# Kernel tuning notes

Measured on AMD Instinct MI355X. Metric: run time of the kernel, lower is better.

Reference implementation:

```python
import jax, jax.numpy as jnp
import numpy as np

B, SX, SY, D = 32, 2048, 2048, 160

def setup_inputs() -> dict:
    key = jax.random.key(0)
    ks = jax.random.split(key, 5)
    s = 1.0 / np.sqrt(D)
    return {
        "x": jax.random.normal(ks[0], (B, SX, D), dtype=jnp.float32),
        "y": jax.random.normal(ks[1], (B, SY, D), dtype=jnp.float32),
        "Wq": jax.random.normal(ks[2], (D, D), dtype=jnp.float32) * s,
        "bq": jnp.zeros((D,), dtype=jnp.float32),
        "Wk": jax.random.normal(ks[3], (D, D), dtype=jnp.float32) * s,
        "bk": jnp.zeros((D,), dtype=jnp.float32),
        "Wv": jax.random.normal(ks[4], (D, D), dtype=jnp.float32) * s,
        "bv": jnp.zeros((D,), dtype=jnp.float32),
    }

def reference(x, y, Wq, bq, Wk, bk, Wv, bv):
    # torch nn.Linear: out = in @ W.T + b, W is [out_dim, in_dim]
    q = jnp.einsum('bxd,ed->bxe', x, Wq) + bq          # [B,SX,D]
    k = jnp.einsum('byd,ed->bye', y, Wk) + bk          # [B,SY,D]
    v = jnp.einsum('byd,ed->bye', y, Wv) + bv          # [B,SY,D]
    scores = jnp.einsum('bxd,byd->bxy', q, k)          # [B,SX,SY] (no scaling in source)
    attn = jax.nn.softmax(scores, axis=-1)
    out = jnp.einsum('bxy,byd->bxd', attn, v)          # dropout is identity at eval
    return out + x                                     # residual
```

## Files before the change

### kernel.cpp

```cpp
#include <hip/hip_runtime.h>

#define LOG2E 1.44269504088896340736f

typedef _Float16 f16;
typedef __attribute__((ext_vector_type(2))) _Float16 f16x2;
typedef __attribute__((ext_vector_type(4))) _Float16 f16x4;
typedef __attribute__((ext_vector_type(8))) _Float16 f16x8;
typedef __attribute__((ext_vector_type(4))) float f32x4;
typedef __attribute__((ext_vector_type(16))) float f32x16;
typedef __attribute__((ext_vector_type(8))) unsigned short us8;

#define BB 32
#define SSX 2048
#define SSY 2048
#define DD 160
#define M_TOTAL (BB*SSX)

#define PRS 168
#define VTRS 136
#define RS 168

__device__ __forceinline__ f32x4 mfma16(f16x8 a, f16x8 b, f32x4 c) {
  return __builtin_amdgcn_mfma_f32_16x16x32_f16(a, b, c, 0, 0, 0);
}

__device__ __forceinline__ f32x16 mfma32(f16x8 a, f16x8 b, f32x16 c) {
  return __builtin_amdgcn_mfma_f32_32x32x16_f16(a, b, c, 0, 0, 0);
}

__device__ __forceinline__ unsigned pk2(float a, float b) {
  union { f16x2 h; unsigned u; } x;
  x.h = (f16x2){(f16)a, (f16)b};
  return x.u;
}

__global__ __launch_bounds__(256, 3) void proj_kernel(
    const float* __restrict__ x, const float* __restrict__ y,
    const float* __restrict__ Wq, const float* __restrict__ bq,
    const float* __restrict__ Wk, const float* __restrict__ bk,
    const float* __restrict__ Wv, const float* __restrict__ bv,
    f16* __restrict__ Qw, f16* __restrict__ Kw, f16* __restrict__ Vtw)
{
  __shared__ __align__(16) f16 buf[160*PRS];
  const int t = threadIdx.x;
  const int wave = t >> 6;
  const int lane = t & 63;
  const int quad = lane >> 4;
  const int l16  = lane & 15;
  const int bid  = (blockIdx.x & 7) * 192 + (blockIdx.x >> 3);
  const int kind = bid % 3;
  const int tile = bid / 3;
  const int row0 = tile * 128;
  const float* src  = (kind == 0) ? x  : y;
  const float* W    = (kind == 0) ? Wq : (kind == 1 ? Wk : Wv);
  const float* bias = (kind == 0) ? bq : (kind == 1 ? bk : bv);

  for (int i = 0; i < 20; ++i) {
    int idx = t + i*256;
    int r = idx / 40, c4 = idx % 40;
    float4 v = *(const float4*)&src[(size_t)(row0 + r)*DD + c4*4];
    f16x4 h = { (f16)v.x, (f16)v.y, (f16)v.z, (f16)v.w };
    *(f16x4*)&buf[r*PRS + c4*4] = h;
  }
  __syncthreads();
  f16x8 afr0[5], afr1[5];
  #pragma unroll
  for (int ks = 0; ks < 5; ++ks) {
    afr0[ks] = *(const f16x8*)&buf[(wave*32 + l16)*PRS + ks*32 + quad*8];
    afr1[ks] = *(const f16x8*)&buf[(wave*32 + 16 + l16)*PRS + ks*32 + quad*8];
  }
  __syncthreads();

  for (int i = 0; i < 25; ++i) {
    int idx = t + i*256;
    int r = idx / 40, c4 = idx % 40;
    float4 v = *(const float4*)&W[r*160 + c4*4];
    f16x4 h = { (f16)v.x, (f16)v.y, (f16)v.z, (f16)v.w };
    *(f16x4*)&buf[r*PRS + c4*4] = h;
  }
  __syncthreads();

  f32x4 acc0[10], acc1[10];
  #pragma unroll
  for (int nt = 0; nt < 10; ++nt) {
    float bs = bias[nt*16 + l16];
    acc0[nt] = (f32x4){bs,bs,bs,bs};
    acc1[nt] = (f32x4){bs,bs,bs,bs};
    #pragma unroll
    for (int ks = 0; ks < 5; ++ks) {
      f16x8 bfr = *(const f16x8*)&buf[(nt*16 + l16)*PRS + ks*32 + quad*8];
      acc0[nt] = mfma16(afr0[ks], bfr, acc0[nt]);
      acc1[nt] = mfma16(afr1[ks], bfr, acc1[nt]);
    }
  }
  __syncthreads();

  if (kind < 2) {
    f16* dst = (kind == 0) ? Qw : Kw;
    #pragma unroll
    for (int nt = 0; nt < 10; ++nt)
      #pragma unroll
      for (int r = 0; r < 4; ++r) {
        buf[(wave*32 + quad*4 + r)*PRS + nt*16 + l16]      = (f16)acc0[nt][r];
        buf[(wave*32 + 16 + quad*4 + r)*PRS + nt*16 + l16] = (f16)acc1[nt][r];
      }
    __syncthreads();
    for (int i = 0; i < 10; ++i) {
      int idx = t + i*256;
      int r = idx / 20, g = idx % 20;
      *(us8*)&dst[(size_t)(row0 + r)*DD + g*8] = *(const us8*)&buf[r*PRS + g*8];
    }
  } else {
    #pragma unroll
    for (int nt = 0; nt < 10; ++nt)
      #pragma unroll
      for (int r = 0; r < 4; ++r) {
        buf[(nt*16 + l16)*VTRS + wave*32 + quad*4 + r]      = (f16)acc0[nt][r];
        buf[(nt*16 + l16)*VTRS + wave*32 + 16 + quad*4 + r] = (f16)acc1[nt][r];
      }
    __syncthreads();
    const int b  = row0 / SSY;
    const int y0 = row0 % SSY;
    for (int i = 0; i < 10; ++i) {
      int idx = t + i*256;
      int d = idx / 16, yg = idx % 16;
      *(us8*)&Vtw[((size_t)b*DD + d)*SSY + y0 + yg*8] = *(const us8*)&buf[d*VTRS + yg*8];
    }
  }
}


#define LOAD_CHUNK(yb) { \
  const f16* ksrc = Kw + ((size_t)b*SSY + (yb))*DD; \
  const f16* vsrc = Vtw + (size_t)b*DD*SSY + (yb); \
  _Pragma("unroll") \
  for (int i = 0; i < 5; ++i) { \
    int idx = t + i*256; int r = idx/20, c = idx%20; \
    kreg[i] = *(const us8*)&ksrc[(size_t)r*DD + c*8]; \
  } \
  _Pragma("unroll") \
  for (int i = 0; i < 5; ++i) { \
    int idx = t + i*256; int d = idx>>3, g = idx&7; \
    vreg[i] = *(const us8*)&vsrc[(size_t)d*SSY + g*8]; \
  } \
}

#define STORE_CHUNK() { \
  _Pragma("unroll") \
  for (int i = 0; i < 5; ++i) { \
    int idx = t + i*256; int r = idx/20, c = idx%20; \
    *(us8*)&K_lds[r*RS + c*8] = kreg[i]; \
  } \
  _Pragma("unroll") \
  for (int i = 0; i < 5; ++i) { \
    int idx = t + i*256; int d = idx>>3, g = idx&7; \
    *(us8*)&Vt_lds[d*64 + ((g ^ (d & 7)) << 3)] = vreg[i]; \
  } \
}

__global__ __launch_bounds__(256, 2) void flash_kernel(
    const f16* __restrict__ Qw, const f16* __restrict__ Kw, const f16* __restrict__ Vtw,
    const float* __restrict__ x, float* __restrict__ out)
{
  __shared__ __align__(16) f16 K_lds[64*RS];
  __shared__ __align__(16) f16 Vt_lds[160*64];
  const int t = threadIdx.x;
  const int wave = t >> 6;
  const int lane = t & 63;
  const int l31  = lane & 31;
  const int hi   = lane >> 5;
  const int bid  = (blockIdx.x & 7) * 64 + (blockIdx.x >> 3);
  const int b    = bid >> 4;
  const int x0   = (bid & 15) * 128;

  us8 kreg[5], vreg[5];
  LOAD_CHUNK(0);

  f16x8 qfr[10];
  #pragma unroll
  for (int h = 0; h < 2; ++h) {
    if (h) __syncthreads();
    const f16* qsrc = Qw + ((size_t)b*SSX + x0 + h*64)*DD;
    for (int i = 0; i < 5; ++i) {
      int idx = t + i*256;
      int r = idx / 20, c = idx % 20;
      *(us8*)&K_lds[r*RS + c*8] = *(const us8*)&qsrc[(size_t)r*DD + c*8];
    }
    __syncthreads();
    if ((wave >> 1) == h) {
      const int base = (wave & 1)*32;
      #pragma unroll
      for (int s = 0; s < 10; ++s)
        qfr[s] = *(const f16x8*)&K_lds[(base + l31)*RS + s*16 + hi*8];
    }
  }

  f32x16 acc[5];
  #pragma unroll
  for (int i = 0; i < 5; ++i)
    #pragma unroll
    for (int r = 0; r < 16; ++r) acc[i][r] = 0.f;
  float m = -1e30f, l = 0.f;

  for (int yc = 0; yc < SSY/64; ++yc) {
    __syncthreads();
    STORE_CHUNK();
    __syncthreads();
    if (yc < SSY/64 - 1) LOAD_CHUNK((yc+1)*64);

    f32x16 S0, S1;
    #pragma unroll
    for (int r = 0; r < 16; ++r) { S0[r] = 0.f; S1[r] = 0.f; }
    __builtin_amdgcn_s_setprio(1);
    #pragma unroll
    for (int s = 0; s < 10; ++s) {
      f16x8 k0 = *(const f16x8*)&K_lds[l31*RS + s*16 + hi*8];
      f16x8 k1 = *(const f16x8*)&K_lds[(32 + l31)*RS + s*16 + hi*8];
      S0 = mfma32(k0, qfr[s], S0);
      S1 = mfma32(k1, qfr[s], S1);
    }
    __builtin_amdgcn_s_setprio(0);

    float pmax = fmaxf(S0[0], S0[1]);
    #pragma unroll
    for (int r = 2; r < 16; r += 2) pmax = fmaxf(pmax, fmaxf(S0[r], S0[r+1]));
    #pragma unroll
    for (int r = 0; r < 16; r += 2) pmax = fmaxf(pmax, fmaxf(S1[r], S1[r+1]));
    pmax = fmaxf(pmax, __shfl_xor(pmax, 32));

    if (__any(pmax > m + 8.f)) {
      float n  = fmaxf(m, pmax);
      float sc = exp2f((m - n)*LOG2E);
      m = n; l *= sc;
      #pragma unroll
      for (int r = 0; r < 16; ++r) {
        float scq = __shfl(sc, (r&3) + 8*(r>>2) + 4*hi);
        #pragma unroll
        for (int dt = 0; dt < 5; ++dt) acc[dt][r] *= scq;
      }
    }

    float lsum = 0.f;
    #pragma unroll
    for (int r = 0; r < 16; ++r) { S0[r] = exp2f((S0[r] - m)*LOG2E); lsum += S0[r]; }
    #pragma unroll
    for (int r = 0; r < 16; ++r) { S1[r] = exp2f((S1[r] - m)*LOG2E); lsum += S1[r]; }
    lsum += __shfl_xor(lsum, 32);
    l += lsum;

    #pragma unroll
    for (int c = 0; c < 4; ++c) {
      const int bo = (c & 1)*8;
      unsigned L0, L1, H0, H1;
      if (c < 2) {
        L0 = pk2(S0[bo+0], S0[bo+1]); L1 = pk2(S0[bo+2], S0[bo+3]);
        H0 = pk2(S0[bo+4], S0[bo+5]); H1 = pk2(S0[bo+6], S0[bo+7]);
      } else {
        L0 = pk2(S1[bo+0], S1[bo+1]); L1 = pk2(S1[bo+2], S1[bo+3]);
        H0 = pk2(S1[bo+4], S1[bo+5]); H1 = pk2(S1[bo+6], S1[bo+7]);
      }
      unsigned sd0 = hi ? L0 : H0;
      unsigned sd1 = hi ? L1 : H1;
      unsigned rc0 = (unsigned)__shfl_xor((int)sd0, 32);
      unsigned rc1 = (unsigned)__shfl_xor((int)sd1, 32);
      union { unsigned u[4]; f16x8 h; } pw;
      pw.u[0] = hi ? rc0 : L0;
      pw.u[1] = hi ? rc1 : L1;
      pw.u[2] = hi ? H0 : rc0;
      pw.u[3] = hi ? H1 : rc1;
      __builtin_amdgcn_s_setprio(1);
      #pragma unroll
      for (int dt = 0; dt < 5; ++dt) {
        int row = dt*32 + l31;
        f16x8 vf = *(const f16x8*)&Vt_lds[row*64 + (((c*2 + hi) ^ (row & 7)) << 3)];
        acc[dt] = mfma32(pw.h, vf, acc[dt]);
      }
      __builtin_amdgcn_s_setprio(0);
    }
  }

  #pragma unroll
  for (int r = 0; r < 16; ++r) {
    int qr = (r&3) + 8*(r>>2) + 4*hi;
    float rl = 1.f / __shfl(l, qr);
    size_t rowoff = ((size_t)b*SSX + x0 + wave*32 + qr)*DD + l31;
    #pragma unroll
    for (int dt = 0; dt < 5; ++dt) {
      size_t o = rowoff + (size_t)dt*32;
      out[o] = acc[dt][r]*rl + x[o];
    }
  }
}

extern "C" void kernel_launch(void* const* d_in, const int* in_sizes, int n_in,
                              void* d_out, int out_size, void* d_ws, size_t ws_size,
                              hipStream_t stream) {
  const float* x  = (const float*)d_in[0];
  const float* y  = (const float*)d_in[1];
  const float* Wq = (const float*)d_in[2];
  const float* bq = (const float*)d_in[3];
  const float* Wk = (const float*)d_in[4];
  const float* bk = (const float*)d_in[5];
  const float* Wv = (const float*)d_in[6];
  const float* bv = (const float*)d_in[7];

  f16* Qw  = (f16*)d_ws;
  f16* Kw  = Qw + (size_t)M_TOTAL*DD;
  f16* Vtw = Kw + (size_t)M_TOTAL*DD;

  proj_kernel<<<1536, 256, 0, stream>>>(x, y, Wq, bq, Wk, bk, Wv, bv, Qw, Kw, Vtw);
  flash_kernel<<<512, 256, 0, stream>>>(Qw, Kw, Vtw, x, (float*)d_out);
}
```

Before: 282.0 us.

## Pre-convert weights, fuse K/V projection per tile, use permlane32 swap and RTZ packing

A small kernel converts the three weight matrices to fp16 once, so projection blocks copy fp16 weights instead of converting fp32 each time. The projection grid drops from 1536 to 1024 blocks, and each y tile now computes both K and V, which removes the redundant reload and conversion of y. In the flash kernel, P packing uses the round-toward-zero packed convert and permlane32_swap in place of select-plus-shuffle. The max reduction is also reordered into a chain. The cost is an extra launch, uneven work between x and y blocks, and slightly different rounding of P.

```diff
diff --git a/kernel.cpp b/kernel.cpp
--- a/kernel.cpp
+++ b/kernel.cpp
@@ -4,11 +4,13 @@
 
 typedef _Float16 f16;
 typedef __attribute__((ext_vector_type(2))) _Float16 f16x2;
+typedef __attribute__((ext_vector_type(2))) __fp16 fp16x2;
 typedef __attribute__((ext_vector_type(4))) _Float16 f16x4;
 typedef __attribute__((ext_vector_type(8))) _Float16 f16x8;
 typedef __attribute__((ext_vector_type(4))) float f32x4;
 typedef __attribute__((ext_vector_type(16))) float f32x16;
 typedef __attribute__((ext_vector_type(8))) unsigned short us8;
+typedef __attribute__((ext_vector_type(2))) int i32x2;
 
 #define BB 32
 #define SSX 2048
@@ -28,17 +30,29 @@
   return __builtin_amdgcn_mfma_f32_32x32x16_f16(a, b, c, 0, 0, 0);
 }
 
-__device__ __forceinline__ unsigned pk2(float a, float b) {
-  union { f16x2 h; unsigned u; } x;
-  x.h = (f16x2){(f16)a, (f16)b};
+__device__ __forceinline__ unsigned pk2rtz(float a, float b) {
+  union { fp16x2 h; unsigned u; } x;
+  x.h = __builtin_amdgcn_cvt_pkrtz(a, b);
   return x.u;
+}
+
+__global__ __launch_bounds__(256) void wcvt_kernel(
+    const float* __restrict__ Wq, const float* __restrict__ Wk, const float* __restrict__ Wv,
+    f16* __restrict__ Wf)
+{
+  int idx = blockIdx.x*256 + threadIdx.x;
+  int which = idx / 6400;
+  int off   = idx % 6400;
+  const float* src = (which == 0) ? Wq : (which == 1 ? Wk : Wv);
+  float4 v = *(const float4*)&src[off*4];
+  f16x4 h = { (f16)v.x, (f16)v.y, (f16)v.z, (f16)v.w };
+  *(f16x4*)&Wf[which*25600 + off*4] = h;
 }
 
 __global__ __launch_bounds__(256, 3) void proj_kernel(
     const float* __restrict__ x, const float* __restrict__ y,
-    const float* __restrict__ Wq, const float* __restrict__ bq,
-    const float* __restrict__ Wk, const float* __restrict__ bk,
-    const float* __restrict__ Wv, const float* __restrict__ bv,
+    const float* __restrict__ bq, const float* __restrict__ bk, const float* __restrict__ bv,
+    const f16* __restrict__ Wf,
     f16* __restrict__ Qw, f16* __restrict__ Kw, f16* __restrict__ Vtw)
 {
   __shared__ __align__(16) f16 buf[160*PRS];
@@ -47,13 +61,11 @@
   const int lane = t & 63;
   const int quad = lane >> 4;
   const int l16  = lane & 15;
-  const int bid  = (blockIdx.x & 7) * 192 + (blockIdx.x >> 3);
-  const int kind = bid % 3;
-  const int tile = bid / 3;
+  const int bid  = (blockIdx.x & 7) * 128 + (blockIdx.x >> 3);
+  const int kind = bid & 1;
+  const int tile = bid >> 1;
   const int row0 = tile * 128;
-  const float* src  = (kind == 0) ? x  : y;
-  const float* W    = (kind == 0) ? Wq : (kind == 1 ? Wk : Wv);
-  const float* bias = (kind == 0) ? bq : (kind == 1 ? bk : bv);
+  const float* src = kind ? y : x;
 
   for (int i = 0; i < 20; ++i) {
     int idx = t + i*256;
@@ -71,32 +83,37 @@
   }
   __syncthreads();
 
-  for (int i = 0; i < 25; ++i) {
-    int idx = t + i*256;
-    int r = idx / 40, c4 = idx % 40;
-    float4 v = *(const float4*)&W[r*160 + c4*4];
-    f16x4 h = { (f16)v.x, (f16)v.y, (f16)v.z, (f16)v.w };
-    *(f16x4*)&buf[r*PRS + c4*4] = h;
-  }
-  __syncthreads();
+#define LOAD_W(mat) { \
+  for (int i = 0; i < 13; ++i) { \
+    int idx = t + i*256; \
+    if (idx < 3200) { \
+      int r = idx / 20, g = idx % 20; \
+      *(us8*)&buf[r*PRS + g*8] = *(const us8*)&Wf[(mat)*25600 + r*160 + g*8]; \
+    } \
+  } }
+
+#define MFMA_PASS(bias) { \
+  _Pragma("unroll") \
+  for (int nt = 0; nt < 10; ++nt) { \
+    float bs = (bias)[nt*16 + l16]; \
+    acc0[nt] = (f32x4){bs,bs,bs,bs}; \
+    acc1[nt] = (f32x4){bs,bs,bs,bs}; \
+    _Pragma("unroll") \
+    for (int ks = 0; ks < 5; ++ks) { \
+      f16x8 bfr = *(const f16x8*)&buf[(nt*16 + l16)*PRS + ks*32 + quad*8]; \
+      acc0[nt] = mfma16(afr0[ks], bfr, acc0[nt]); \
+      acc1[nt] = mfma16(afr1[ks], bfr, acc1[nt]); \
+    } \
+  } }
 
   f32x4 acc0[10], acc1[10];
-  #pragma unroll
-  for (int nt = 0; nt < 10; ++nt) {
-    float bs = bias[nt*16 + l16];
-    acc0[nt] = (f32x4){bs,bs,bs,bs};
-    acc1[nt] = (f32x4){bs,bs,bs,bs};
-    #pragma unroll
-    for (int ks = 0; ks < 5; ++ks) {
-      f16x8 bfr = *(const f16x8*)&buf[(nt*16 + l16)*PRS + ks*32 + quad*8];
-      acc0[nt] = mfma16(afr0[ks], bfr, acc0[nt]);
-      acc1[nt] = mfma16(afr1[ks], bfr, acc1[nt]);
-    }
-  }
-  __syncthreads();
-
-  if (kind < 2) {
-    f16* dst = (kind == 0) ? Qw : Kw;
+
+  LOAD_W(kind ? 1 : 0);
+  __syncthreads();
+  MFMA_PASS(kind ? bk : bq);
+  __syncthreads();
+  {
+    f16* dst = kind ? Kw : Qw;
     #pragma unroll
     for (int nt = 0; nt < 10; ++nt)
       #pragma unroll
@@ -110,7 +127,15 @@
       int r = idx / 20, g = idx % 20;
       *(us8*)&dst[(size_t)(row0 + r)*DD + g*8] = *(const us8*)&buf[r*PRS + g*8];
     }
-  } else {
+  }
+  if (!kind) return;
+
+  __syncthreads();
+  LOAD_W(2);
+  __syncthreads();
+  MFMA_PASS(bv);
+  __syncthreads();
+  {
     #pragma unroll
     for (int nt = 0; nt < 10; ++nt)
       #pragma unroll
@@ -223,9 +248,9 @@
 
     float pmax = fmaxf(S0[0], S0[1]);
     #pragma unroll
-    for (int r = 2; r < 16; r += 2) pmax = fmaxf(pmax, fmaxf(S0[r], S0[r+1]));
-    #pragma unroll
-    for (int r = 0; r < 16; r += 2) pmax = fmaxf(pmax, fmaxf(S1[r], S1[r+1]));
+    for (int r = 2; r < 16; r += 2) pmax = fmaxf(fmaxf(pmax, S0[r]), S0[r+1]);
+    #pragma unroll
+    for (int r = 0; r < 16; r += 2) pmax = fmaxf(fmaxf(pmax, S1[r]), S1[r+1]);
     pmax = fmaxf(pmax, __shfl_xor(pmax, 32));
 
     if (__any(pmax > m + 8.f)) {
@@ -251,29 +276,27 @@
     #pragma unroll
     for (int c = 0; c < 4; ++c) {
       const int bo = (c & 1)*8;
-      unsigned L0, L1, H0, H1;
-      if (c < 2) {
-        L0 = pk2(S0[bo+0], S0[bo+1]); L1 = pk2(S0[bo+2], S0[bo+3]);
-        H0 = pk2(S0[bo+4], S0[bo+5]); H1 = pk2(S0[bo+6], S0[bo+7]);
-      } else {
-        L0 = pk2(S1[bo+0], S1[bo+1]); L1 = pk2(S1[bo+2], S1[bo+3]);
-        H0 = pk2(S1[bo+4], S1[bo+5]); H1 = pk2(S1[bo+6], S1[bo+7]);
-      }
-      unsigned sd0 = hi ? L0 : H0;
-      unsigned sd1 = hi ? L1 : H1;
-      unsigned rc0 = (unsigned)__shfl_xor((int)sd0, 32);
-      unsigned rc1 = (unsigned)__shfl_xor((int)sd1, 32);
-      union { unsigned u[4]; f16x8 h; } pw;
-      pw.u[0] = hi ? rc0 : L0;
-      pw.u[1] = hi ? rc1 : L1;
-      pw.u[2] = hi ? H0 : rc0;
-      pw.u[3] = hi ? H1 : rc1;
+      float s0 = (c < 2) ? S0[bo+0] : S1[bo+0];
+      float s1 = (c < 2) ? S0[bo+1] : S1[bo+1];
+      float s2 = (c < 2) ? S0[bo+2] : S1[bo+2];
+      float s3 = (c < 2) ? S0[bo+3] : S1[bo+3];
+      float s4 = (c < 2) ? S0[bo+4] : S1[bo+4];
+      float s5 = (c < 2) ? S0[bo+5] : S1[bo+5];
+      float s6 = (c < 2) ? S0[bo+6] : S1[bo+6];
+      float s7 = (c < 2) ? S0[bo+7] : S1[bo+7];
+      unsigned L0 = pk2rtz(s0, s1), L1 = pk2rtz(s2, s3);
+      unsigned H0 = pk2rtz(s4, s5), H1 = pk2rtz(s6, s7);
+      i32x2 r02 = __builtin_amdgcn_permlane32_swap((int)L0, (int)H0, false, false);
+      i32x2 r13 = __builtin_amdgcn_permlane32_swap((int)L1, (int)H1, false, false);
+      union { unsigned u[4]; f16x8 h; } ph;
+      ph.u[0] = (unsigned)r02.x; ph.u[1] = (unsigned)r13.x;
+      ph.u[2] = (unsigned)r02.y; ph.u[3] = (unsigned)r13.y;
       __builtin_amdgcn_s_setprio(1);
       #pragma unroll
       for (int dt = 0; dt < 5; ++dt) {
         int row = dt*32 + l31;
         f16x8 vf = *(const f16x8*)&Vt_lds[row*64 + (((c*2 + hi) ^ (row & 7)) << 3)];
-        acc[dt] = mfma32(pw.h, vf, acc[dt]);
+        acc[dt] = mfma32(ph.h, vf, acc[dt]);
       }
       __builtin_amdgcn_s_setprio(0);
     }
@@ -307,7 +330,10 @@
   f16* Qw  = (f16*)d_ws;
   f16* Kw  = Qw + (size_t)M_TOTAL*DD;
   f16* Vtw = Kw + (size_t)M_TOTAL*DD;
-
-  proj_kernel<<<1536, 256, 0, stream>>>(x, y, Wq, bq, Wk, bk, Wv, bv, Qw, Kw, Vtw);
+  size_t wf_off = (ws_size - 153600) & ~(size_t)255;
+  f16* Wf = (f16*)((char*)d_ws + wf_off);
+
+  wcvt_kernel<<<75, 256, 0, stream>>>(Wq, Wk, Wv, Wf);
+  proj_kernel<<<1024, 256, 0, stream>>>(x, y, bq, bk, bv, Wf, Qw, Kw, Vtw);
   flash_kernel<<<512, 256, 0, stream>>>(Qw, Kw, Vtw, x, (float*)d_out);
 }
```

Result: slower. 290.3 us (+2.9%).
